# Performance work log

Hardware: AMD Instinct MI355X
Metric: run time of the kernel (lower is better)

## Reference

```python
import jax, jax.numpy as jnp
import numpy as np

N_NODES = 100000
N_EDGES = 800000
IN_DIM = 128
HID = 128


def setup_inputs() -> dict:
    key = jax.random.key(0)
    ks = jax.random.split(key, 8)
    s = 0.05
    x = jax.random.normal(ks[0], (N_NODES, IN_DIM), jnp.float32)
    edge_index = jax.random.randint(ks[1], (2, N_EDGES), 0, N_NODES)
    return {
        "x": x,
        "edge_index": edge_index,
        "W1l": jax.random.normal(ks[2], (HID, IN_DIM), jnp.float32) * s,
        "b1l": jnp.zeros((HID,), jnp.float32),
        "W1r": jax.random.normal(ks[3], (HID, IN_DIM), jnp.float32) * s,
        "W2l": jax.random.normal(ks[4], (HID, HID), jnp.float32) * s,
        "b2l": jnp.zeros((HID,), jnp.float32),
        "W2r": jax.random.normal(ks[5], (HID, HID), jnp.float32) * s,
        "Wm1": jax.random.normal(ks[6], (HID, 2 * HID), jnp.float32) * s,
        "bm1": jnp.zeros((HID,), jnp.float32),
        "Wm2": jax.random.normal(ks[7], (1, HID), jnp.float32) * s,
        "bm2": jnp.zeros((1,), jnp.float32),
    }


def sage_conv(x, src, dst, Wl, bl, Wr):
    # PyG SAGEConv (mean aggr): out = lin_l(mean_{j in N(i)} x_j) + lin_r(x_i)
    msg = x[src]  # [E, d] gather of source features
    agg = jax.ops.segment_sum(msg, dst, num_segments=N_NODES)  # [N, d]
    deg = jax.ops.segment_sum(jnp.ones((src.shape[0],), x.dtype), dst, num_segments=N_NODES)
    agg = agg / jnp.maximum(deg, 1.0)[:, None]
    return agg @ Wl.T + bl + x @ Wr.T


def reference(x, edge_index, W1l, b1l, W1r, W2l, b2l, W2r, Wm1, bm1, Wm2, bm2):
    src, dst = edge_index[0], edge_index[1]
    h = jax.nn.relu(sage_conv(x, src, dst, W1l, b1l, W1r))  # dropout = identity (eval)
    h = jax.nn.relu(sage_conv(h, src, dst, W2l, b2l, W2r))
    ef = jnp.concatenate([h[src], h[dst]], axis=1)  # [E, 2*HID]
    hidden = jax.nn.relu(ef @ Wm1.T + bm1)  # [E, HID]
    logits = (hidden @ Wm2.T + bm2)[:, 0]  # [E]
    return jax.nn.sigmoid(logits)
```

## Files before the change

kernel.cpp:

```cpp
#include <hip/hip_runtime.h>
#include <math.h>

#define NN 100000
#define NE 800000
#define D 128

typedef __attribute__((ext_vector_type(8))) short bf16x8;
typedef __attribute__((ext_vector_type(8))) unsigned short u16x8;
typedef __attribute__((ext_vector_type(4))) float f32x4;

constexpr size_t OFF_RS  = 0;
constexpr size_t OFF_CNT = 512 * 1024;
constexpr size_t OFF_CUR = 1024 * 1024;
constexpr size_t OFF_BS  = 1536 * 1024;
constexpr size_t OFF_WB  = 1552 * 1024;
constexpr size_t OFF_SRC = 2 * 1024 * 1024;
constexpr size_t OFF_EID = 6 * 1024 * 1024;
constexpr size_t OFF_B0  = 10 * 1024 * 1024;
constexpr size_t OFF_B2  = OFF_B0 + 26 * 1024 * 1024;
constexpr size_t OFF_B3  = OFF_B2 + 26 * 1024 * 1024;

__device__ __forceinline__ unsigned short f2b(float f) {
    unsigned u = __builtin_bit_cast(unsigned, f);
    return (unsigned short)((u + 0x7FFFu + ((u >> 16) & 1u)) >> 16);
}
__device__ __forceinline__ float b2f(unsigned short h) {
    unsigned u = ((unsigned)h) << 16;
    return __builtin_bit_cast(float, u);
}

__global__ __launch_bounds__(256) void k_prep(const float* __restrict__ x,
                                              unsigned short* __restrict__ xb,
                                              const float* __restrict__ W1l,
                                              const float* __restrict__ W1r,
                                              const float* __restrict__ W2l,
                                              const float* __restrict__ W2r,
                                              const float* __restrict__ Wm1,
                                              unsigned short* __restrict__ wb,
                                              const int* __restrict__ dst,
                                              int* __restrict__ cnt) {
    int bid = blockIdx.x, tid = threadIdx.x;
    if (bid < 12500) {
        int i = bid * 256 + tid;
        float4 v = *(const float4*)&x[(size_t)i * 4];
        ushort4 o;
        o.x = f2b(v.x); o.y = f2b(v.y); o.z = f2b(v.z); o.w = f2b(v.w);
        *(ushort4*)&xb[(size_t)i * 4] = o;
    } else if (bid < 12884) {
        int i = (bid - 12500) * 256 + tid;
        float v;
        if (i < 16384) v = W1l[i];
        else if (i < 32768) v = W1r[i - 16384];
        else if (i < 49152) v = W2l[i - 32768];
        else if (i < 65536) v = W2r[i - 49152];
        else v = Wm1[i - 65536];
        wb[i] = f2b(v);
    } else {
        int e = (bid - 12884) * 256 + tid;
        atomicAdd(&cnt[dst[e]], 1);
    }
}

__global__ __launch_bounds__(256) void k_scan1(const int* __restrict__ cnt,
                                               int* __restrict__ bsum) {
    int i = blockIdx.x * 256 + threadIdx.x;
    int v = (i < NN) ? cnt[i] : 0;
    #pragma unroll
    for (int o = 1; o < 64; o <<= 1) v += __shfl_xor(v, o);
    __shared__ int wsum[4];
    if ((threadIdx.x & 63) == 0) wsum[threadIdx.x >> 6] = v;
    __syncthreads();
    if (threadIdx.x == 0) bsum[blockIdx.x] = wsum[0] + wsum[1] + wsum[2] + wsum[3];
}

__global__ __launch_bounds__(512) void k_scan2(int* __restrict__ bsum, int nb) {
    __shared__ int s[512];
    int t = threadIdx.x;
    int v = (t < nb) ? bsum[t] : 0;
    s[t] = v;
    __syncthreads();
    for (int o = 1; o < 512; o <<= 1) {
        int u = (t >= o) ? s[t - o] : 0;
        __syncthreads();
        s[t] += u;
        __syncthreads();
    }
    if (t < nb) bsum[t] = s[t] - v;
}

__global__ __launch_bounds__(256) void k_scan3(const int* __restrict__ cnt,
                                               const int* __restrict__ bsum,
                                               int* __restrict__ rs,
                                               int* __restrict__ cur) {
    __shared__ int s[256];
    int t = threadIdx.x;
    int i = blockIdx.x * 256 + t;
    int v = (i < NN) ? cnt[i] : 0;
    s[t] = v;
    __syncthreads();
    for (int o = 1; o < 256; o <<= 1) {
        int u = (t >= o) ? s[t - o] : 0;
        __syncthreads();
        s[t] += u;
        __syncthreads();
    }
    int ex = s[t] - v + bsum[blockIdx.x];
    if (i < NN) { rs[i] = ex; cur[i] = ex; }
    if (i == NN - 1) rs[NN] = ex + v;
}

__global__ __launch_bounds__(256) void k_scatter_idx(const int* __restrict__ src,
                                                     const int* __restrict__ dst,
                                                     int* __restrict__ cur,
                                                     int* __restrict__ srcs,
                                                     int* __restrict__ eids) {
    int e = blockIdx.x * 256 + threadIdx.x;
    if (e < NE) {
        int pos = atomicAdd(&cur[dst[e]], 1);
        srcs[pos] = src[e];
        eids[pos] = e;
    }
}

__device__ __forceinline__ void gather_mean64(const unsigned short* __restrict__ feat,
                                              const int* __restrict__ rs,
                                              const int* __restrict__ re,
                                              const int* __restrict__ srcs,
                                              int n0, unsigned short* agt) {
    const int tid = threadIdx.x;
    const int g = tid >> 4, q = tid & 15;
    #pragma unroll
    for (int half = 0; half < 2; ++half) {
        int r = half * 32 + g;
        int n = n0 + r;
        if (n > NN - 1) n = NN - 1;
        int b = rs[n], e = re[n];
        float a0[8] = {}, a1[8] = {}, a2[8] = {}, a3[8] = {};
        int j = b;
        for (; j + 7 < e; j += 8) {
            int s0 = srcs[j],     s1 = srcs[j + 1], s2 = srcs[j + 2], s3 = srcs[j + 3];
            int s4 = srcs[j + 4], s5 = srcs[j + 5], s6 = srcs[j + 6], s7 = srcs[j + 7];
            u16x8 v0 = *(const u16x8*)&feat[(size_t)s0 * D + q * 8];
            u16x8 v1 = *(const u16x8*)&feat[(size_t)s1 * D + q * 8];
            u16x8 v2 = *(const u16x8*)&feat[(size_t)s2 * D + q * 8];
            u16x8 v3 = *(const u16x8*)&feat[(size_t)s3 * D + q * 8];
            u16x8 v4 = *(const u16x8*)&feat[(size_t)s4 * D + q * 8];
            u16x8 v5 = *(const u16x8*)&feat[(size_t)s5 * D + q * 8];
            u16x8 v6 = *(const u16x8*)&feat[(size_t)s6 * D + q * 8];
            u16x8 v7 = *(const u16x8*)&feat[(size_t)s7 * D + q * 8];
            #pragma unroll
            for (int i = 0; i < 8; ++i) a0[i] += b2f(v0[i]) + b2f(v4[i]);
            #pragma unroll
            for (int i = 0; i < 8; ++i) a1[i] += b2f(v1[i]) + b2f(v5[i]);
            #pragma unroll
            for (int i = 0; i < 8; ++i) a2[i] += b2f(v2[i]) + b2f(v6[i]);
            #pragma unroll
            for (int i = 0; i < 8; ++i) a3[i] += b2f(v3[i]) + b2f(v7[i]);
        }
        for (; j + 3 < e; j += 4) {
            int s0 = srcs[j], s1 = srcs[j + 1], s2 = srcs[j + 2], s3 = srcs[j + 3];
            u16x8 v0 = *(const u16x8*)&feat[(size_t)s0 * D + q * 8];
            u16x8 v1 = *(const u16x8*)&feat[(size_t)s1 * D + q * 8];
            u16x8 v2 = *(const u16x8*)&feat[(size_t)s2 * D + q * 8];
            u16x8 v3 = *(const u16x8*)&feat[(size_t)s3 * D + q * 8];
            #pragma unroll
            for (int i = 0; i < 8; ++i) a0[i] += b2f(v0[i]);
            #pragma unroll
            for (int i = 0; i < 8; ++i) a1[i] += b2f(v1[i]);
            #pragma unroll
            for (int i = 0; i < 8; ++i) a2[i] += b2f(v2[i]);
            #pragma unroll
            for (int i = 0; i < 8; ++i) a3[i] += b2f(v3[i]);
        }
        for (; j < e; ++j) {
            int s0 = srcs[j];
            u16x8 v0 = *(const u16x8*)&feat[(size_t)s0 * D + q * 8];
            #pragma unroll
            for (int i = 0; i < 8; ++i) a0[i] += b2f(v0[i]);
        }
        float inv = 1.0f / fmaxf((float)(e - b), 1.0f);
        u16x8 o;
        #pragma unroll
        for (int i = 0; i < 8; ++i) o[i] = f2b((a0[i] + a1[i] + a2[i] + a3[i]) * inv);
        *(u16x8*)&agt[r * 136 + q * 8] = o;
    }
}

__device__ __forceinline__ void stage_tile(const unsigned short* __restrict__ src,
                                           int n0, unsigned short* t) {
    const int tid = threadIdx.x;
    #pragma unroll
    for (int it = 0; it < 2; ++it) {
        int idx = it * 512 + tid;
        int r = idx >> 4, c = (idx & 15) * 8;
        int gr = n0 + r;
        if (gr > NN - 1) gr = NN - 1;
        *(u16x8*)&t[r * 136 + c] = *(const u16x8*)&src[(size_t)gr * D + c];
    }
}

__device__ __forceinline__ void store_tile(const unsigned short* t,
                                           int n0, unsigned short* __restrict__ dstp) {
    const int tid = threadIdx.x;
    #pragma unroll
    for (int it = 0; it < 2; ++it) {
        int idx = it * 512 + tid;
        int r = idx >> 4, c = (idx & 15) * 8;
        int gr = n0 + r;
        if (gr < NN)
            *(u16x8*)&dstp[(size_t)gr * D + c] = *(const u16x8*)&t[r * 136 + c];
    }
}

__global__ __launch_bounds__(512) void k_aggconv1(const unsigned short* __restrict__ xb,
                                                  const int* __restrict__ rs,
                                                  const int* __restrict__ re,
                                                  const int* __restrict__ srcs,
                                                  const unsigned short* __restrict__ Wlb,
                                                  const unsigned short* __restrict__ Wrb,
                                                  const float* __restrict__ bias,
                                                  unsigned short* __restrict__ hout) {
    __shared__ unsigned short agt[64 * 136];
    __shared__ unsigned short sto[64 * 136];
    const int tid = threadIdx.x;
    const int n0 = blockIdx.x * 64;

    stage_tile(xb, n0, sto);
    gather_mean64(xb, rs, re, srcs, n0, agt);
    __syncthreads();

    const int wv = tid >> 6, l = tid & 63;
    const int lrow = l & 15, lk = (l >> 4) * 8;
    f32x4 acc[4] = {};
    #pragma unroll
    for (int p = 0; p < 2; ++p) {
        const unsigned short* W  = p ? Wrb : Wlb;
        const unsigned short* At = p ? sto : agt;
        #pragma unroll
        for (int ks = 0; ks < 4; ++ks) {
            bf16x8 bfr = *(const bf16x8*)&W[(size_t)(wv * 16 + lrow) * D + ks * 32 + lk];
            #pragma unroll
            for (int mt = 0; mt < 4; ++mt) {
                bf16x8 af = *(const bf16x8*)&At[(mt * 16 + lrow) * 136 + ks * 32 + lk];
                acc[mt] = __builtin_amdgcn_mfma_f32_16x16x32_bf16(af, bfr, acc[mt], 0, 0, 0);
            }
        }
    }
    __syncthreads();
    const int orow = (l >> 4) * 4, ocol = l & 15;
    float bb = bias[wv * 16 + ocol];
    #pragma unroll
    for (int mt = 0; mt < 4; ++mt)
        #pragma unroll
        for (int j = 0; j < 4; ++j)
            sto[(mt * 16 + orow + j) * 136 + wv * 16 + ocol] =
                f2b(fmaxf(acc[mt][j] + bb, 0.0f));
    __syncthreads();
    store_tile(sto, n0, hout);
}

__global__ __launch_bounds__(512) void k_aggconv2uv(const unsigned short* __restrict__ h1b,
                                                    const int* __restrict__ rs,
                                                    const int* __restrict__ re,
                                                    const int* __restrict__ srcs,
                                                    const unsigned short* __restrict__ Wlb,
                                                    const unsigned short* __restrict__ Wrb,
                                                    const float* __restrict__ bias,
                                                    const unsigned short* __restrict__ Wm1b,
                                                    const float* __restrict__ bm1,
                                                    unsigned short* __restrict__ Ub,
                                                    unsigned short* __restrict__ Vb) {
    __shared__ unsigned short agt[64 * 136];
    __shared__ unsigned short sto[64 * 136];
    const int tid = threadIdx.x;
    const int n0 = blockIdx.x * 64;

    stage_tile(h1b, n0, sto);
    gather_mean64(h1b, rs, re, srcs, n0, agt);
    __syncthreads();

    const int wv = tid >> 6, l = tid & 63;
    const int lrow = l & 15, lk = (l >> 4) * 8;
    const int orow = (l >> 4) * 4, ocol = l & 15;

    f32x4 acc[4] = {};
    #pragma unroll
    for (int p = 0; p < 2; ++p) {
        const unsigned short* W  = p ? Wrb : Wlb;
        const unsigned short* At = p ? sto : agt;
        #pragma unroll
        for (int ks = 0; ks < 4; ++ks) {
            bf16x8 bfr = *(const bf16x8*)&W[(size_t)(wv * 16 + lrow) * D + ks * 32 + lk];
            #pragma unroll
            for (int mt = 0; mt < 4; ++mt) {
                bf16x8 af = *(const bf16x8*)&At[(mt * 16 + lrow) * 136 + ks * 32 + lk];
                acc[mt] = __builtin_amdgcn_mfma_f32_16x16x32_bf16(af, bfr, acc[mt], 0, 0, 0);
            }
        }
    }
    __syncthreads();
    {
        float bb = bias[wv * 16 + ocol];
        #pragma unroll
        for (int mt = 0; mt < 4; ++mt)
            #pragma unroll
            for (int j = 0; j < 4; ++j)
                agt[(mt * 16 + orow + j) * 136 + wv * 16 + ocol] =
                    f2b(fmaxf(acc[mt][j] + bb, 0.0f));
    }
    __syncthreads();

    f32x4 aU[4] = {}, aV[4] = {};
    #pragma unroll
    for (int ks = 0; ks < 4; ++ks) {
        bf16x8 bu = *(const bf16x8*)&Wm1b[(size_t)(wv * 16 + lrow) * 256 + ks * 32 + lk];
        bf16x8 bv = *(const bf16x8*)&Wm1b[(size_t)(wv * 16 + lrow) * 256 + 128 + ks * 32 + lk];
        #pragma unroll
        for (int mt = 0; mt < 4; ++mt) {
            bf16x8 af = *(const bf16x8*)&agt[(mt * 16 + lrow) * 136 + ks * 32 + lk];
            aU[mt] = __builtin_amdgcn_mfma_f32_16x16x32_bf16(af, bu, aU[mt], 0, 0, 0);
            aV[mt] = __builtin_amdgcn_mfma_f32_16x16x32_bf16(af, bv, aV[mt], 0, 0, 0);
        }
    }
    {
        float bb = bm1[wv * 16 + ocol];
        #pragma unroll
        for (int mt = 0; mt < 4; ++mt)
            #pragma unroll
            for (int j = 0; j < 4; ++j)
                sto[(mt * 16 + orow + j) * 136 + wv * 16 + ocol] = f2b(aU[mt][j] + bb);
    }
    __syncthreads();
    store_tile(sto, n0, Ub);
    {
        #pragma unroll
        for (int mt = 0; mt < 4; ++mt)
            #pragma unroll
            for (int j = 0; j < 4; ++j)
                agt[(mt * 16 + orow + j) * 136 + wv * 16 + ocol] = f2b(aV[mt][j]);
    }
    __syncthreads();
    store_tile(agt, n0, Vb);
}

__global__ __launch_bounds__(256) void k_edge2(const unsigned short* __restrict__ Ub,
                                               const unsigned short* __restrict__ Vb,
                                               const int* __restrict__ rs,
                                               const int* __restrict__ re,
                                               const int* __restrict__ srcs,
                                               const int* __restrict__ eids,
                                               const float* __restrict__ wm2,
                                               const float* __restrict__ bm2,
                                               float* __restrict__ out) {
    int t = blockIdx.x * 256 + threadIdx.x;
    int g = t >> 4, q = t & 15;
    if (g >= NN) return;
    int b = rs[g], e = re[g];
    if (b == e) return;
    u16x8 vv = *(const u16x8*)&Vb[(size_t)g * D + q * 8];
    float vf[8], wf[8];
    #pragma unroll
    for (int i = 0; i < 8; ++i) vf[i] = b2f(vv[i]);
    float4 w0 = *(const float4*)&wm2[q * 8];
    float4 w1 = *(const float4*)&wm2[q * 8 + 4];
    wf[0] = w0.x; wf[1] = w0.y; wf[2] = w0.z; wf[3] = w0.w;
    wf[4] = w1.x; wf[5] = w1.y; wf[6] = w1.z; wf[7] = w1.w;
    const float bb = bm2[0];

    int j = b;
    for (; j + 7 < e; j += 8) {
        u16x8 u0 = *(const u16x8*)&Ub[(size_t)srcs[j]     * D + q * 8];
        u16x8 u1 = *(const u16x8*)&Ub[(size_t)srcs[j + 1] * D + q * 8];
        u16x8 u2 = *(const u16x8*)&Ub[(size_t)srcs[j + 2] * D + q * 8];
        u16x8 u3 = *(const u16x8*)&Ub[(size_t)srcs[j + 3] * D + q * 8];
        u16x8 u4 = *(const u16x8*)&Ub[(size_t)srcs[j + 4] * D + q * 8];
        u16x8 u5 = *(const u16x8*)&Ub[(size_t)srcs[j + 5] * D + q * 8];
        u16x8 u6 = *(const u16x8*)&Ub[(size_t)srcs[j + 6] * D + q * 8];
        u16x8 u7 = *(const u16x8*)&Ub[(size_t)srcs[j + 7] * D + q * 8];
        float p0 = 0.f, p1 = 0.f, p2 = 0.f, p3 = 0.f;
        float p4 = 0.f, p5 = 0.f, p6 = 0.f, p7 = 0.f;
        #pragma unroll
        for (int i = 0; i < 8; ++i) {
            p0 += fmaxf(b2f(u0[i]) + vf[i], 0.0f) * wf[i];
            p1 += fmaxf(b2f(u1[i]) + vf[i], 0.0f) * wf[i];
            p2 += fmaxf(b2f(u2[i]) + vf[i], 0.0f) * wf[i];
            p3 += fmaxf(b2f(u3[i]) + vf[i], 0.0f) * wf[i];
            p4 += fmaxf(b2f(u4[i]) + vf[i], 0.0f) * wf[i];
            p5 += fmaxf(b2f(u5[i]) + vf[i], 0.0f) * wf[i];
            p6 += fmaxf(b2f(u6[i]) + vf[i], 0.0f) * wf[i];
            p7 += fmaxf(b2f(u7[i]) + vf[i], 0.0f) * wf[i];
        }
        #pragma unroll
        for (int off = 1; off < 16; off <<= 1) {
            p0 += __shfl_xor(p0, off); p1 += __shfl_xor(p1, off);
            p2 += __shfl_xor(p2, off); p3 += __shfl_xor(p3, off);
            p4 += __shfl_xor(p4, off); p5 += __shfl_xor(p5, off);
            p6 += __shfl_xor(p6, off); p7 += __shfl_xor(p7, off);
        }
        if (q == 0) {
            out[eids[j]]     = 1.0f / (1.0f + expf(-(p0 + bb)));
            out[eids[j + 1]] = 1.0f / (1.0f + expf(-(p1 + bb)));
            out[eids[j + 2]] = 1.0f / (1.0f + expf(-(p2 + bb)));
            out[eids[j + 3]] = 1.0f / (1.0f + expf(-(p3 + bb)));
            out[eids[j + 4]] = 1.0f / (1.0f + expf(-(p4 + bb)));
            out[eids[j + 5]] = 1.0f / (1.0f + expf(-(p5 + bb)));
            out[eids[j + 6]] = 1.0f / (1.0f + expf(-(p6 + bb)));
            out[eids[j + 7]] = 1.0f / (1.0f + expf(-(p7 + bb)));
        }
    }
    for (; j + 3 < e; j += 4) {
        u16x8 u0 = *(const u16x8*)&Ub[(size_t)srcs[j]     * D + q * 8];
        u16x8 u1 = *(const u16x8*)&Ub[(size_t)srcs[j + 1] * D + q * 8];
        u16x8 u2 = *(const u16x8*)&Ub[(size_t)srcs[j + 2] * D + q * 8];
        u16x8 u3 = *(const u16x8*)&Ub[(size_t)srcs[j + 3] * D + q * 8];
        float p0 = 0.f, p1 = 0.f, p2 = 0.f, p3 = 0.f;
        #pragma unroll
        for (int i = 0; i < 8; ++i) {
            p0 += fmaxf(b2f(u0[i]) + vf[i], 0.0f) * wf[i];
            p1 += fmaxf(b2f(u1[i]) + vf[i], 0.0f) * wf[i];
            p2 += fmaxf(b2f(u2[i]) + vf[i], 0.0f) * wf[i];
            p3 += fmaxf(b2f(u3[i]) + vf[i], 0.0f) * wf[i];
        }
        #pragma unroll
        for (int off = 1; off < 16; off <<= 1) {
            p0 += __shfl_xor(p0, off); p1 += __shfl_xor(p1, off);
            p2 += __shfl_xor(p2, off); p3 += __shfl_xor(p3, off);
        }
        if (q == 0) {
            out[eids[j]]     = 1.0f / (1.0f + expf(-(p0 + bb)));
            out[eids[j + 1]] = 1.0f / (1.0f + expf(-(p1 + bb)));
            out[eids[j + 2]] = 1.0f / (1.0f + expf(-(p2 + bb)));
            out[eids[j + 3]] = 1.0f / (1.0f + expf(-(p3 + bb)));
        }
    }
    for (; j < e; ++j) {
        u16x8 u0 = *(const u16x8*)&Ub[(size_t)srcs[j] * D + q * 8];
        float p0 = 0.f;
        #pragma unroll
        for (int i = 0; i < 8; ++i) p0 += fmaxf(b2f(u0[i]) + vf[i], 0.0f) * wf[i];
        #pragma unroll
        for (int off = 1; off < 16; off <<= 1) p0 += __shfl_xor(p0, off);
        if (q == 0) out[eids[j]] = 1.0f / (1.0f + expf(-(p0 + bb)));
    }
}

extern "C" void kernel_launch(void* const* d_in, const int* in_sizes, int n_in,
                              void* d_out, int out_size, void* d_ws, size_t ws_size,
                              hipStream_t stream) {
    const float* x   = (const float*)d_in[0];
    const int*   ei  = (const int*)d_in[1];
    const int*   src = ei;
    const int*   dst = ei + NE;
    const float* W1l = (const float*)d_in[2];
    const float* b1l = (const float*)d_in[3];
    const float* W1r = (const float*)d_in[4];
    const float* W2l = (const float*)d_in[5];
    const float* b2l = (const float*)d_in[6];
    const float* W2r = (const float*)d_in[7];
    const float* Wm1 = (const float*)d_in[8];
    const float* bm1 = (const float*)d_in[9];
    const float* Wm2 = (const float*)d_in[10];
    const float* bm2 = (const float*)d_in[11];
    float* out = (float*)d_out;

    char* ws = (char*)d_ws;
    int* rs   = (int*)(ws + OFF_RS);
    int* cnt  = (int*)(ws + OFF_CNT);
    int* cur  = (int*)(ws + OFF_CUR);
    int* bsum = (int*)(ws + OFF_BS);
    unsigned short* wb = (unsigned short*)(ws + OFF_WB);
    int* srcs = (int*)(ws + OFF_SRC);
    int* eids = (int*)(ws + OFF_EID);
    unsigned short* B0 = (unsigned short*)(ws + OFF_B0);
    unsigned short* B2 = (unsigned short*)(ws + OFF_B2);
    unsigned short* B3 = (unsigned short*)(ws + OFF_B3);

    unsigned short* W1lb = wb;
    unsigned short* W1rb = wb + 16384;
    unsigned short* W2lb = wb + 32768;
    unsigned short* W2rb = wb + 49152;
    unsigned short* Wm1b = wb + 65536;

    const int NB = 391;
    const int NB64 = (NN + 63) / 64;

    hipMemsetAsync(cnt, 0, NN * sizeof(int), stream);
    k_prep<<<12500 + 384 + 3125, 256, 0, stream>>>(x, B0, W1l, W1r, W2l, W2r, Wm1,
                                                   wb, dst, cnt);
    k_scan1<<<NB, 256, 0, stream>>>(cnt, bsum);
    k_scan2<<<1, 512, 0, stream>>>(bsum, NB);
    k_scan3<<<NB, 256, 0, stream>>>(cnt, bsum, rs, cur);
    k_scatter_idx<<<(NE + 255) / 256, 256, 0, stream>>>(src, dst, cur, srcs, eids);

    k_aggconv1<<<NB64, 512, 0, stream>>>(B0, rs, cur, srcs, W1lb, W1rb, b1l, B2);
    k_aggconv2uv<<<NB64, 512, 0, stream>>>(B2, rs, cur, srcs, W2lb, W2rb, b2l,
                                           Wm1b, bm1, B3, B0);
    k_edge2<<<(NN * 16 + 255) / 256, 256, 0, stream>>>(B3, B0, rs, cur, srcs, eids,
                                                       Wm2, bm2, out);
}
```

Before: 288.4 us.

## Store gathered node features in FP8 to halve random-gather traffic

Adds FP8 (e4m3) copies of x, the layer-1 output and the U edge-projection, written alongside the bf16 tiles. The three neighbour-gather phases (both mean aggregations and the edge scoring) now read 8-byte FP8 chunks instead of 16-byte bf16 ones and unpack them with packed cvt instructions. The aim is to cut memory traffic in the bandwidth-bound scattered gathers. In exchange it adds extra FP8 writes and lowers precision, which may push the outputs beyond tolerance.

New measurement: 283.7 us. About the same (-1.6%).

```diff
diff --git a/kernel.cpp b/kernel.cpp
--- a/kernel.cpp
+++ b/kernel.cpp
@@ -8,6 +8,7 @@
 typedef __attribute__((ext_vector_type(8))) short bf16x8;
 typedef __attribute__((ext_vector_type(8))) unsigned short u16x8;
 typedef __attribute__((ext_vector_type(4))) float f32x4;
+typedef __attribute__((ext_vector_type(2))) float f32x2;
 
 constexpr size_t OFF_RS  = 0;
 constexpr size_t OFF_CNT = 512 * 1024;
@@ -18,7 +19,9 @@
 constexpr size_t OFF_EID = 6 * 1024 * 1024;
 constexpr size_t OFF_B0  = 10 * 1024 * 1024;
 constexpr size_t OFF_B2  = OFF_B0 + 26 * 1024 * 1024;
-constexpr size_t OFF_B3  = OFF_B2 + 26 * 1024 * 1024;
+constexpr size_t OFF_X8  = OFF_B2 + 26 * 1024 * 1024;
+constexpr size_t OFF_H8  = OFF_X8 + 13 * 1024 * 1024;
+constexpr size_t OFF_U8  = OFF_H8 + 13 * 1024 * 1024;
 
 __device__ __forceinline__ unsigned short f2b(float f) {
     unsigned u = __builtin_bit_cast(unsigned, f);
@@ -31,6 +34,7 @@
 
 __global__ __launch_bounds__(256) void k_prep(const float* __restrict__ x,
                                               unsigned short* __restrict__ xb,
+                                              unsigned* __restrict__ x8w,
                                               const float* __restrict__ W1l,
                                               const float* __restrict__ W1r,
                                               const float* __restrict__ W2l,
@@ -46,6 +50,9 @@
         ushort4 o;
         o.x = f2b(v.x); o.y = f2b(v.y); o.z = f2b(v.z); o.w = f2b(v.w);
         *(ushort4*)&xb[(size_t)i * 4] = o;
+        unsigned p = __builtin_amdgcn_cvt_pk_fp8_f32(v.x, v.y, 0u, false);
+        p = __builtin_amdgcn_cvt_pk_fp8_f32(v.z, v.w, p, true);
+        x8w[i] = p;
     } else if (bid < 12884) {
         int i = (bid - 12500) * 256 + tid;
         float v;
@@ -122,7 +129,15 @@
     }
 }
 
-__device__ __forceinline__ void gather_mean64(const unsigned short* __restrict__ feat,
+#define UNPK8(acc, u) {                                               \
+    f32x2 p0 = __builtin_amdgcn_cvt_pk_f32_fp8(u.x, false);           \
+    f32x2 p1 = __builtin_amdgcn_cvt_pk_f32_fp8(u.x, true);            \
+    f32x2 p2 = __builtin_amdgcn_cvt_pk_f32_fp8(u.y, false);           \
+    f32x2 p3 = __builtin_amdgcn_cvt_pk_f32_fp8(u.y, true);            \
+    acc[0] += p0.x; acc[1] += p0.y; acc[2] += p1.x; acc[3] += p1.y;   \
+    acc[4] += p2.x; acc[5] += p2.y; acc[6] += p3.x; acc[7] += p3.y; }
+
+__device__ __forceinline__ void gather_mean64(const unsigned char* __restrict__ feat8,
                                               const int* __restrict__ rs,
                                               const int* __restrict__ re,
                                               const int* __restrict__ srcs,
@@ -138,45 +153,27 @@
         float a0[8] = {}, a1[8] = {}, a2[8] = {}, a3[8] = {};
         int j = b;
         for (; j + 7 < e; j += 8) {
-            int s0 = srcs[j],     s1 = srcs[j + 1], s2 = srcs[j + 2], s3 = srcs[j + 3];
-            int s4 = srcs[j + 4], s5 = srcs[j + 5], s6 = srcs[j + 6], s7 = srcs[j + 7];
-            u16x8 v0 = *(const u16x8*)&feat[(size_t)s0 * D + q * 8];
-            u16x8 v1 = *(const u16x8*)&feat[(size_t)s1 * D + q * 8];
-            u16x8 v2 = *(const u16x8*)&feat[(size_t)s2 * D + q * 8];
-            u16x8 v3 = *(const u16x8*)&feat[(size_t)s3 * D + q * 8];
-            u16x8 v4 = *(const u16x8*)&feat[(size_t)s4 * D + q * 8];
-            u16x8 v5 = *(const u16x8*)&feat[(size_t)s5 * D + q * 8];
-            u16x8 v6 = *(const u16x8*)&feat[(size_t)s6 * D + q * 8];
-            u16x8 v7 = *(const u16x8*)&feat[(size_t)s7 * D + q * 8];
-            #pragma unroll
-            for (int i = 0; i < 8; ++i) a0[i] += b2f(v0[i]) + b2f(v4[i]);
-            #pragma unroll
-            for (int i = 0; i < 8; ++i) a1[i] += b2f(v1[i]) + b2f(v5[i]);
-            #pragma unroll
-            for (int i = 0; i < 8; ++i) a2[i] += b2f(v2[i]) + b2f(v6[i]);
-            #pragma unroll
-            for (int i = 0; i < 8; ++i) a3[i] += b2f(v3[i]) + b2f(v7[i]);
+            uint2 v0 = *(const uint2*)&feat8[(size_t)srcs[j]     * 128 + q * 8];
+            uint2 v1 = *(const uint2*)&feat8[(size_t)srcs[j + 1] * 128 + q * 8];
+            uint2 v2 = *(const uint2*)&feat8[(size_t)srcs[j + 2] * 128 + q * 8];
+            uint2 v3 = *(const uint2*)&feat8[(size_t)srcs[j + 3] * 128 + q * 8];
+            uint2 v4 = *(const uint2*)&feat8[(size_t)srcs[j + 4] * 128 + q * 8];
+            uint2 v5 = *(const uint2*)&feat8[(size_t)srcs[j + 5] * 128 + q * 8];
+            uint2 v6 = *(const uint2*)&feat8[(size_t)srcs[j + 6] * 128 + q * 8];
+            uint2 v7 = *(const uint2*)&feat8[(size_t)srcs[j + 7] * 128 + q * 8];
+            UNPK8(a0, v0); UNPK8(a1, v1); UNPK8(a2, v2); UNPK8(a3, v3);
+            UNPK8(a0, v4); UNPK8(a1, v5); UNPK8(a2, v6); UNPK8(a3, v7);
         }
         for (; j + 3 < e; j += 4) {
-            int s0 = srcs[j], s1 = srcs[j + 1], s2 = srcs[j + 2], s3 = srcs[j + 3];
-            u16x8 v0 = *(const u16x8*)&feat[(size_t)s0 * D + q * 8];
-            u16x8 v1 = *(const u16x8*)&feat[(size_t)s1 * D + q * 8];
-            u16x8 v2 = *(const u16x8*)&feat[(size_t)s2 * D + q * 8];
-            u16x8 v3 = *(const u16x8*)&feat[(size_t)s3 * D + q * 8];
-            #pragma unroll
-            for (int i = 0; i < 8; ++i) a0[i] += b2f(v0[i]);
-            #pragma unroll
-            for (int i = 0; i < 8; ++i) a1[i] += b2f(v1[i]);
-            #pragma unroll
-            for (int i = 0; i < 8; ++i) a2[i] += b2f(v2[i]);
-            #pragma unroll
-            for (int i = 0; i < 8; ++i) a3[i] += b2f(v3[i]);
+            uint2 v0 = *(const uint2*)&feat8[(size_t)srcs[j]     * 128 + q * 8];
+            uint2 v1 = *(const uint2*)&feat8[(size_t)srcs[j + 1] * 128 + q * 8];
+            uint2 v2 = *(const uint2*)&feat8[(size_t)srcs[j + 2] * 128 + q * 8];
+            uint2 v3 = *(const uint2*)&feat8[(size_t)srcs[j + 3] * 128 + q * 8];
+            UNPK8(a0, v0); UNPK8(a1, v1); UNPK8(a2, v2); UNPK8(a3, v3);
         }
         for (; j < e; ++j) {
-            int s0 = srcs[j];
-            u16x8 v0 = *(const u16x8*)&feat[(size_t)s0 * D + q * 8];
-            #pragma unroll
-            for (int i = 0; i < 8; ++i) a0[i] += b2f(v0[i]);
+            uint2 v0 = *(const uint2*)&feat8[(size_t)srcs[j] * 128 + q * 8];
+            UNPK8(a0, v0);
         }
         float inv = 1.0f / fmaxf((float)(e - b), 1.0f);
         u16x8 o;
@@ -212,21 +209,41 @@
     }
 }
 
+__device__ __forceinline__ void store_tile_fp8(const unsigned short* t,
+                                               int n0, unsigned char* __restrict__ dst8) {
+    const int tid = threadIdx.x;
+    #pragma unroll
+    for (int it = 0; it < 4; ++it) {
+        int w = it * 512 + tid;
+        int r = w >> 5, c4 = (w & 31) * 4;
+        int gr = n0 + r;
+        if (gr < NN) {
+            unsigned p = __builtin_amdgcn_cvt_pk_fp8_f32(
+                b2f(t[r * 136 + c4 + 0]), b2f(t[r * 136 + c4 + 1]), 0u, false);
+            p = __builtin_amdgcn_cvt_pk_fp8_f32(
+                b2f(t[r * 136 + c4 + 2]), b2f(t[r * 136 + c4 + 3]), p, true);
+            *(unsigned*)&dst8[(size_t)gr * 128 + c4] = p;
+        }
+    }
+}
+
 __global__ __launch_bounds__(512) void k_aggconv1(const unsigned short* __restrict__ xb,
+                                                  const unsigned char* __restrict__ x8,
                                                   const int* __restrict__ rs,
                                                   const int* __restrict__ re,
                                                   const int* __restrict__ srcs,
                                                   const unsigned short* __restrict__ Wlb,
                                                   const unsigned short* __restrict__ Wrb,
                                                   const float* __restrict__ bias,
-                                                  unsigned short* __restrict__ hout) {
+                                                  unsigned short* __restrict__ hout,
+                                                  unsigned char* __restrict__ h8) {
     __shared__ unsigned short agt[64 * 136];
     __shared__ unsigned short sto[64 * 136];
     const int tid = threadIdx.x;
     const int n0 = blockIdx.x * 64;
 
     stage_tile(xb, n0, sto);
-    gather_mean64(xb, rs, re, srcs, n0, agt);
+    gather_mean64(x8, rs, re, srcs, n0, agt);
     __syncthreads();
 
     const int wv = tid >> 6, l = tid & 63;
@@ -257,9 +274,11 @@
                 f2b(fmaxf(acc[mt][j] + bb, 0.0f));
     __syncthreads();
     store_tile(sto, n0, hout);
+    store_tile_fp8(sto, n0, h8);
 }
 
 __global__ __launch_bounds__(512) void k_aggconv2uv(const unsigned short* __restrict__ h1b,
+                                                    const unsigned char* __restrict__ h8,
                                                     const int* __restrict__ rs,
                                                     const int* __restrict__ re,
                                                     const int* __restrict__ srcs,
@@ -268,7 +287,7 @@
                                                     const float* __restrict__ bias,
                                                     const unsigned short* __restrict__ Wm1b,
                                                     const float* __restrict__ bm1,
-                                                    unsigned short* __restrict__ Ub,
+                                                    unsigned char* __restrict__ U8,
                                                     unsigned short* __restrict__ Vb) {
     __shared__ unsigned short agt[64 * 136];
     __shared__ unsigned short sto[64 * 136];
@@ -276,7 +295,7 @@
     const int n0 = blockIdx.x * 64;
 
     stage_tile(h1b, n0, sto);
-    gather_mean64(h1b, rs, re, srcs, n0, agt);
+    gather_mean64(h8, rs, re, srcs, n0, agt);
     __syncthreads();
 
     const int wv = tid >> 6, l = tid & 63;
@@ -331,7 +350,7 @@
                 sto[(mt * 16 + orow + j) * 136 + wv * 16 + ocol] = f2b(aU[mt][j] + bb);
     }
     __syncthreads();
-    store_tile(sto, n0, Ub);
+    store_tile_fp8(sto, n0, U8);
     {
         #pragma unroll
         for (int mt = 0; mt < 4; ++mt)
@@ -343,7 +362,7 @@
     store_tile(agt, n0, Vb);
 }
 
-__global__ __launch_bounds__(256) void k_edge2(const unsigned short* __restrict__ Ub,
+__global__ __launch_bounds__(256) void k_edge2(const unsigned char* __restrict__ U8,
                                                const unsigned short* __restrict__ Vb,
                                                const int* __restrict__ rs,
                                                const int* __restrict__ re,
@@ -367,29 +386,30 @@
     wf[4] = w1.x; wf[5] = w1.y; wf[6] = w1.z; wf[7] = w1.w;
     const float bb = bm2[0];
 
+#define EDOT(p, u) {                                                   \
+    f32x2 q0 = __builtin_amdgcn_cvt_pk_f32_fp8(u.x, false);            \
+    f32x2 q1 = __builtin_amdgcn_cvt_pk_f32_fp8(u.x, true);             \
+    f32x2 q2 = __builtin_amdgcn_cvt_pk_f32_fp8(u.y, false);            \
+    f32x2 q3 = __builtin_amdgcn_cvt_pk_f32_fp8(u.y, true);             \
+    p += fmaxf(q0.x + vf[0], 0.0f) * wf[0] + fmaxf(q0.y + vf[1], 0.0f) * wf[1] \
+       + fmaxf(q1.x + vf[2], 0.0f) * wf[2] + fmaxf(q1.y + vf[3], 0.0f) * wf[3] \
+       + fmaxf(q2.x + vf[4], 0.0f) * wf[4] + fmaxf(q2.y + vf[5], 0.0f) * wf[5] \
+       + fmaxf(q3.x + vf[6], 0.0f) * wf[6] + fmaxf(q3.y + vf[7], 0.0f) * wf[7]; }
+
     int j = b;
     for (; j + 7 < e; j += 8) {
-        u16x8 u0 = *(const u16x8*)&Ub[(size_t)srcs[j]     * D + q * 8];
-        u16x8 u1 = *(const u16x8*)&Ub[(size_t)srcs[j + 1] * D + q * 8];
-        u16x8 u2 = *(const u16x8*)&Ub[(size_t)srcs[j + 2] * D + q * 8];
-        u16x8 u3 = *(const u16x8*)&Ub[(size_t)srcs[j + 3] * D + q * 8];
-        u16x8 u4 = *(const u16x8*)&Ub[(size_t)srcs[j + 4] * D + q * 8];
-        u16x8 u5 = *(const u16x8*)&Ub[(size_t)srcs[j + 5] * D + q * 8];
-        u16x8 u6 = *(const u16x8*)&Ub[(size_t)srcs[j + 6] * D + q * 8];
-        u16x8 u7 = *(const u16x8*)&Ub[(size_t)srcs[j + 7] * D + q * 8];
+        uint2 u0 = *(const uint2*)&U8[(size_t)srcs[j]     * 128 + q * 8];
+        uint2 u1 = *(const uint2*)&U8[(size_t)srcs[j + 1] * 128 + q * 8];
+        uint2 u2 = *(const uint2*)&U8[(size_t)srcs[j + 2] * 128 + q * 8];
+        uint2 u3 = *(const uint2*)&U8[(size_t)srcs[j + 3] * 128 + q * 8];
+        uint2 u4 = *(const uint2*)&U8[(size_t)srcs[j + 4] * 128 + q * 8];
+        uint2 u5 = *(const uint2*)&U8[(size_t)srcs[j + 5] * 128 + q * 8];
+        uint2 u6 = *(const uint2*)&U8[(size_t)srcs[j + 6] * 128 + q * 8];
+        uint2 u7 = *(const uint2*)&U8[(size_t)srcs[j + 7] * 128 + q * 8];
         float p0 = 0.f, p1 = 0.f, p2 = 0.f, p3 = 0.f;
         float p4 = 0.f, p5 = 0.f, p6 = 0.f, p7 = 0.f;
-        #pragma unroll
-        for (int i = 0; i < 8; ++i) {
-            p0 += fmaxf(b2f(u0[i]) + vf[i], 0.0f) * wf[i];
-            p1 += fmaxf(b2f(u1[i]) + vf[i], 0.0f) * wf[i];
-            p2 += fmaxf(b2f(u2[i]) + vf[i], 0.0f) * wf[i];
-            p3 += fmaxf(b2f(u3[i]) + vf[i], 0.0f) * wf[i];
-            p4 += fmaxf(b2f(u4[i]) + vf[i], 0.0f) * wf[i];
-            p5 += fmaxf(b2f(u5[i]) + vf[i], 0.0f) * wf[i];
-            p6 += fmaxf(b2f(u6[i]) + vf[i], 0.0f) * wf[i];
-            p7 += fmaxf(b2f(u7[i]) + vf[i], 0.0f) * wf[i];
-        }
+        EDOT(p0, u0); EDOT(p1, u1); EDOT(p2, u2); EDOT(p3, u3);
+        EDOT(p4, u4); EDOT(p5, u5); EDOT(p6, u6); EDOT(p7, u7);
         #pragma unroll
         for (int off = 1; off < 16; off <<= 1) {
             p0 += __shfl_xor(p0, off); p1 += __shfl_xor(p1, off);
@@ -409,18 +429,12 @@
         }
     }
     for (; j + 3 < e; j += 4) {
-        u16x8 u0 = *(const u16x8*)&Ub[(size_t)srcs[j]     * D + q * 8];
-        u16x8 u1 = *(const u16x8*)&Ub[(size_t)srcs[j + 1] * D + q * 8];
-        u16x8 u2 = *(const u16x8*)&Ub[(size_t)srcs[j + 2] * D + q * 8];
-        u16x8 u3 = *(const u16x8*)&Ub[(size_t)srcs[j + 3] * D + q * 8];
+        uint2 u0 = *(const uint2*)&U8[(size_t)srcs[j]     * 128 + q * 8];
+        uint2 u1 = *(const uint2*)&U8[(size_t)srcs[j + 1] * 128 + q * 8];
+        uint2 u2 = *(const uint2*)&U8[(size_t)srcs[j + 2] * 128 + q * 8];
+        uint2 u3 = *(const uint2*)&U8[(size_t)srcs[j + 3] * 128 + q * 8];
         float p0 = 0.f, p1 = 0.f, p2 = 0.f, p3 = 0.f;
-        #pragma unroll
-        for (int i = 0; i < 8; ++i) {
-            p0 += fmaxf(b2f(u0[i]) + vf[i], 0.0f) * wf[i];
-            p1 += fmaxf(b2f(u1[i]) + vf[i], 0.0f) * wf[i];
-            p2 += fmaxf(b2f(u2[i]) + vf[i], 0.0f) * wf[i];
-            p3 += fmaxf(b2f(u3[i]) + vf[i], 0.0f) * wf[i];
-        }
+        EDOT(p0, u0); EDOT(p1, u1); EDOT(p2, u2); EDOT(p3, u3);
         #pragma unroll
         for (int off = 1; off < 16; off <<= 1) {
             p0 += __shfl_xor(p0, off); p1 += __shfl_xor(p1, off);
@@ -434,10 +448,9 @@
         }
     }
     for (; j < e; ++j) {
-        u16x8 u0 = *(const u16x8*)&Ub[(size_t)srcs[j] * D + q * 8];
+        uint2 u0 = *(const uint2*)&U8[(size_t)srcs[j] * 128 + q * 8];
         float p0 = 0.f;
-        #pragma unroll
-        for (int i = 0; i < 8; ++i) p0 += fmaxf(b2f(u0[i]) + vf[i], 0.0f) * wf[i];
+        EDOT(p0, u0);
         #pragma unroll
         for (int off = 1; off < 16; off <<= 1) p0 += __shfl_xor(p0, off);
         if (q == 0) out[eids[j]] = 1.0f / (1.0f + expf(-(p0 + bb)));
@@ -473,7 +486,9 @@
     int* eids = (int*)(ws + OFF_EID);
     unsigned short* B0 = (unsigned short*)(ws + OFF_B0);
     unsigned short* B2 = (unsigned short*)(ws + OFF_B2);
-    unsigned short* B3 = (unsigned short*)(ws + OFF_B3);
+    unsigned char*  X8 = (unsigned char*)(ws + OFF_X8);
+    unsigned char*  H8 = (unsigned char*)(ws + OFF_H8);
+    unsigned char*  U8 = (unsigned char*)(ws + OFF_U8);
 
     unsigned short* W1lb = wb;
     unsigned short* W1rb = wb + 16384;
@@ -485,16 +500,19 @@
     const int NB64 = (NN + 63) / 64;
 
     hipMemsetAsync(cnt, 0, NN * sizeof(int), stream);
-    k_prep<<<12500 + 384 + 3125, 256, 0, stream>>>(x, B0, W1l, W1r, W2l, W2r, Wm1,
+    k_prep<<<12500 + 384 + 3125, 256, 0, stream>>>(x, B0, (unsigned*)X8,
+                                                   W1l, W1r, W2l, W2r, Wm1,
                                                    wb, dst, cnt);
     k_scan1<<<NB, 256, 0, stream>>>(cnt, bsum);
     k_scan2<<<1, 512, 0, stream>>>(bsum, NB);
     k_scan3<<<NB, 256, 0, stream>>>(cnt, bsum, rs, cur);
     k_scatter_idx<<<(NE + 255) / 256, 256, 0, stream>>>(src, dst, cur, srcs, eids);
 
-    k_aggconv1<<<NB64, 512, 0, stream>>>(B0, rs, cur, srcs, W1lb, W1rb, b1l, B2);
-    k_aggconv2uv<<<NB64, 512, 0, stream>>>(B2, rs, cur, srcs, W2lb, W2rb, b2l,
-                                           Wm1b, bm1, B3, B0);
-    k_edge2<<<(NN * 16 + 255) / 256, 256, 0, stream>>>(B3, B0, rs, cur, srcs, eids,
+    k_aggconv1<<<NB64, 512, 0, stream>>>(B0, X8, rs, cur, srcs,
+                                         W1lb, W1rb, b1l, B2, H8);
+    k_aggconv2uv<<<NB64, 512, 0, stream>>>(B2, H8, rs, cur, srcs,
+                                           W2lb, W2rb, b2l, Wm1b, bm1,
+                                           U8, B0);
+    k_edge2<<<(NN * 16 + 255) / 256, 256, 0, stream>>>(U8, B0, rs, cur, srcs, eids,
                                                        Wm2, bm2, out);
 }
```
